# Kernel optimization log

Hardware: AMD Instinct MI355X
Metric: run time of the kernel (lower is better)

The kernel has to match this reference:

```python
import jax, jax.numpy as jnp
import numpy as np

B, S, F, RANK = 8, 4096, 1024, 64


def gram_schmidt(P):
    """Sequential Gram-Schmidt on columns of P (F, R) -> orthogonal (unnormalized) columns.
    Matches vizbert's orth_tensor: v_i = p_i - sum_{j<i} ((u_j . v)/(u_j . u_j)) u_j.
    Each step vectorizes the inner projection loop as one matmul (u_j are mutually
    orthogonal, so sequential-update and batched coefficients are equal in exact math)."""
    us = [P[:, 0]]
    for i in range(1, P.shape[1]):
        U = jnp.stack(us, axis=1)                 # (F, i)
        sq = jnp.sum(U * U, axis=0)               # (i,)
        v = P[:, i]
        coeff = (U.T @ v) / sq                    # (i,)
        us.append(v - U @ coeff)
    return jnp.stack(us, axis=1)                  # (F, R)


def setup_inputs() -> dict:
    key = jax.random.key(0)
    k1, k2 = jax.random.split(key)
    hidden_states = jax.random.normal(k1, (B, S, F), dtype=jnp.float32)
    # probe params initialized uniform(-0.05, 0.05), stacked to (num_features, rank)
    probe = jax.random.uniform(k2, (F, RANK), minval=-0.05, maxval=0.05, dtype=jnp.float32)
    return {"hidden_states": hidden_states, "probe": probe}


def reference(hidden_states, probe):
    # orth_probe: Gram-Schmidt orthogonalized probe columns (orthogonalize=True)
    U = gram_schmidt(probe)                       # (F, R), orthogonal columns
    sq = jnp.sum(U * U, axis=0)                   # (R,) squared norms

    # normalize=True: remember per-token norms before projection
    old_norms = jnp.linalg.norm(hidden_states, axis=2, keepdims=True)  # (B, S, 1)
    # mask_first=True: remember first-token states
    first_state = hidden_states[:, 0]             # (B, F)

    # full_batch_gs: subtract projection onto each probe direction.
    # Because U's columns are orthogonal, the sequential per-column subtraction
    # equals one fused projection: h - U (U^T h / ||u||^2).
    coeffs = jnp.einsum('bsf,fr->bsr', hidden_states, U) / sq
    h = hidden_states - jnp.einsum('bsr,fr->bsf', coeffs, U)

    # normalize=True: rescale back to the original per-token norm
    new_norms = jnp.linalg.norm(h, axis=2, keepdims=True)
    h = h / new_norms * old_norms

    # mask_first=True: restore the first token untouched
    h = h.at[:, 0].set(first_state)
    return h
```

## Files before the change

### kernel.cpp

```cpp
#include <hip/hip_runtime.h>


typedef __attribute__((ext_vector_type(8))) short bf16x8;
typedef __attribute__((ext_vector_type(4))) float f32x4;

#define MFMA_B16(a, b, c) __builtin_amdgcn_mfma_f32_16x16x32_bf16((a), (b), (c), 0, 0, 0)

__device__ __forceinline__ unsigned short bf16bits(float x) {
  union { float f; unsigned u; } v; v.f = x;
  return (unsigned short)((v.u + 0x7fffu + ((v.u >> 16) & 1u)) >> 16);
}

__global__ void pp_gram(const float* __restrict__ P, float* __restrict__ partial,
                        unsigned short* __restrict__ Ptb, unsigned short* __restrict__ Pb) {
  __shared__ float Pl[64][68];
  const int tid = threadIdx.x, ch = blockIdx.x;
  #pragma unroll
  for (int u = 0; u < 4; ++u) {
    const int f = tid >> 2, r = (tid & 3) * 16 + 4 * u;
    *(f32x4*)&Pl[f][r] = *(const f32x4*)(P + (size_t)(ch * 64 + f) * 64 + r);
  }
  __syncthreads();
  {
    const int f = tid >> 2, r0 = (tid & 3) * 16;
    bf16x8 w0, w1;
    #pragma unroll
    for (int j = 0; j < 8; ++j) {
      w0[j] = (short)bf16bits(Pl[f][r0 + j]);
      w1[j] = (short)bf16bits(Pl[f][r0 + 8 + j]);
    }
    *(bf16x8*)(Pb + (size_t)(ch * 64 + f) * 64 + r0) = w0;
    *(bf16x8*)(Pb + (size_t)(ch * 64 + f) * 64 + r0 + 8) = w1;
  }
  {
    const int r = tid >> 2, f0 = (tid & 3) * 16;
    bf16x8 w0, w1;
    #pragma unroll
    for (int j = 0; j < 8; ++j) {
      w0[j] = (short)bf16bits(Pl[f0 + j][r]);
      w1[j] = (short)bf16bits(Pl[f0 + 8 + j][r]);
    }
    *(bf16x8*)(Ptb + (size_t)r * 1024 + ch * 64 + f0) = w0;
    *(bf16x8*)(Ptb + (size_t)r * 1024 + ch * 64 + f0 + 8) = w1;
  }
  const int a0 = (tid >> 4) * 4, b0 = (tid & 15) * 4;
  f32x4 acc[4];
  #pragma unroll
  for (int i = 0; i < 4; ++i) acc[i] = (f32x4){0.f, 0.f, 0.f, 0.f};
  for (int k = 0; k < 64; ++k) {
    f32x4 av = *(const f32x4*)&Pl[k][a0];
    f32x4 bv = *(const f32x4*)&Pl[k][b0];
    #pragma unroll
    for (int i = 0; i < 4; ++i) acc[i] += av[i] * bv;
  }
  #pragma unroll
  for (int i = 0; i < 4; ++i)
    *(f32x4*)(partial + (size_t)ch * 4096 + (size_t)(a0 + i) * 64 + b0) = acc[i];
}

__global__ void pp_invert(const float* __restrict__ partial, unsigned short* __restrict__ Wb) {
  __shared__ float A[64][68];
  const int i = threadIdx.x;
  #pragma unroll
  for (int c = 0; c < 16; ++c) {
    f32x4 s = (f32x4){0.f, 0.f, 0.f, 0.f};
    #pragma unroll 4
    for (int p = 0; p < 16; ++p)
      s += *(const f32x4*)(partial + (size_t)p * 4096 + (size_t)i * 64 + c * 4);
    *(f32x4*)&A[i][c * 4] = s;
  }
  __syncthreads();
  for (int k = 0; k < 64; ++k) {
    const float d = 1.0f / A[k][k];
    const float fi = A[i][k];
    #pragma unroll
    for (int c = 0; c < 16; ++c) {
      f32x4 pr = *(const f32x4*)&A[k][c * 4];
      f32x4 cur = *(const f32x4*)&A[i][c * 4];
      f32x4 res;
      #pragma unroll
      for (int e = 0; e < 4; ++e) {
        const bool isp = (c * 4 + e) == k;
        const float pv = isp ? d : pr[e] * d;
        const float cu = isp ? 0.f : cur[e];
        res[e] = (i == k) ? pv : (cu - fi * pv);
      }
      *(f32x4*)&A[i][c * 4] = res;
    }
    __builtin_amdgcn_wave_barrier();
  }
  #pragma unroll
  for (int c = 0; c < 8; ++c) {
    bf16x8 w;
    #pragma unroll
    for (int j = 0; j < 8; ++j) w[j] = (short)bf16bits(A[i][c * 8 + j]);
    *(bf16x8*)(Wb + (size_t)i * 64 + c * 8) = w;
  }
}

__device__ __forceinline__ void ld_chunk(const float* __restrict__ hp, int ch, f32x4* v) {
  #pragma unroll
  for (int it = 0; it < 4; ++it) {
    v[2 * it] = *(const f32x4*)(hp + ch * 128 + it * 32);
    v[2 * it + 1] = *(const f32x4*)(hp + ch * 128 + it * 32 + 4);
  }
}

__device__ __forceinline__ void comp_chunk(const f32x4* v, const unsigned short* __restrict__ bp0,
                                           int ch, f32x4* accY, float& sqacc) {
  #pragma unroll
  for (int it = 0; it < 4; ++it) {
    const f32x4 v0 = v[2 * it], v1 = v[2 * it + 1];
    sqacc += v0[0] * v0[0] + v0[1] * v0[1] + v0[2] * v0[2] + v0[3] * v0[3] +
             v1[0] * v1[0] + v1[1] * v1[1] + v1[2] * v1[2] + v1[3] * v1[3];
    bf16x8 a;
    a[0] = (short)bf16bits(v0[0]); a[1] = (short)bf16bits(v0[1]);
    a[2] = (short)bf16bits(v0[2]); a[3] = (short)bf16bits(v0[3]);
    a[4] = (short)bf16bits(v1[0]); a[5] = (short)bf16bits(v1[1]);
    a[6] = (short)bf16bits(v1[2]); a[7] = (short)bf16bits(v1[3]);
    const unsigned short* bp = bp0 + ch * 128 + it * 32;
    #pragma unroll
    for (int t = 0; t < 4; ++t) {
      bf16x8 b = *(const bf16x8*)(bp + (size_t)t * 16 * 1024);
      accY[t] = MFMA_B16(a, b, accY[t]);
    }
  }
}

__global__ __launch_bounds__(256, 2) void pp_main(
    const float* __restrict__ H, const unsigned short* __restrict__ Ptb,
    const unsigned short* __restrict__ Pb, const unsigned short* __restrict__ Wb,
    float* __restrict__ out) {
  __shared__ __align__(16) unsigned short Yl[64][72];
  __shared__ __align__(16) unsigned short Cl[64][72];
  __shared__ __align__(16) unsigned short Wl[64][72];

  const int tid = threadIdx.x;
  const int lane = tid & 63, wid = tid >> 6;
  const int c16 = lane & 15, quad = lane >> 4;
  const int strip = wid * 16;
  const long row0 = (long)blockIdx.x * 64;

  #pragma unroll
  for (int g = 0; g < 2; ++g) {
    const int u = tid + g * 256;
    *(bf16x8*)&Wl[u >> 3][(u & 7) * 8] = *(const bf16x8*)(Wb + (size_t)u * 8);
  }
  __syncthreads();

  f32x4 accY[4];
  #pragma unroll
  for (int t = 0; t < 4; ++t) accY[t] = (f32x4){0.f, 0.f, 0.f, 0.f};
  float sqacc = 0.f;
  const float* hp = H + (row0 + strip + c16) * 1024 + quad * 8;
  const unsigned short* bp0 = Ptb + (size_t)c16 * 1024 + quad * 8;
  {
    f32x4 va[8], vb[8];
    ld_chunk(hp, 0, va);
    #pragma unroll
    for (int c2 = 0; c2 < 4; ++c2) {
      ld_chunk(hp, 2 * c2 + 1, vb);
      comp_chunk(va, bp0, 2 * c2, accY, sqacc);
      if (c2 < 3) ld_chunk(hp, 2 * c2 + 2, va);
      comp_chunk(vb, bp0, 2 * c2 + 1, accY, sqacc);
    }
  }

  sqacc += __shfl_xor(sqacc, 16);
  sqacc += __shfl_xor(sqacc, 32);

  #pragma unroll
  for (int t = 0; t < 4; ++t)
    #pragma unroll
    for (int r = 0; r < 4; ++r)
      Yl[strip + quad * 4 + r][t * 16 + c16] = bf16bits(accY[t][r]);

  f32x4 accC[4];
  #pragma unroll
  for (int t = 0; t < 4; ++t) accC[t] = (f32x4){0.f, 0.f, 0.f, 0.f};
  #pragma unroll
  for (int kk = 0; kk < 2; ++kk) {
    bf16x8 a = *(const bf16x8*)&Yl[strip + c16][kk * 32 + quad * 8];
    #pragma unroll
    for (int t = 0; t < 4; ++t) {
      bf16x8 b = *(const bf16x8*)&Wl[t * 16 + c16][kk * 32 + quad * 8];
      accC[t] = MFMA_B16(a, b, accC[t]);
    }
  }

  #pragma unroll
  for (int t = 0; t < 4; ++t)
    #pragma unroll
    for (int r = 0; r < 4; ++r)
      Cl[strip + quad * 4 + r][t * 16 + c16] = bf16bits(accC[t][r]);

  float sc[4]; long rg[4]; bool fs[4];
  #pragma unroll
  for (int r = 0; r < 4; ++r) {
    float dd = accY[0][r] * accC[0][r] + accY[1][r] * accC[1][r] +
               accY[2][r] * accC[2][r] + accY[3][r] * accC[3][r];
    dd += __shfl_xor(dd, 1);
    dd += __shfl_xor(dd, 2);
    dd += __shfl_xor(dd, 4);
    dd += __shfl_xor(dd, 8);
    const float o2 = __shfl(sqacc, quad * 4 + r);
    const float n2 = fmaxf(o2 - dd, 1e-30f);
    sc[r] = sqrtf(o2 / n2);
    rg[r] = row0 + strip + quad * 4 + r;
    fs[r] = ((rg[r] & 4095) == 0);
  }

  bf16x8 ca0 = *(const bf16x8*)&Cl[strip + c16][quad * 8];
  bf16x8 ca1 = *(const bf16x8*)&Cl[strip + c16][32 + quad * 8];
  #pragma unroll 4
  for (int ft = 0; ft < 64; ++ft) {
    const unsigned short* bp = Pb + (size_t)(ft * 16 + c16) * 64 + quad * 8;
    bf16x8 b0 = *(const bf16x8*)bp;
    bf16x8 b1 = *(const bf16x8*)(bp + 32);
    f32x4 acc = (f32x4){0.f, 0.f, 0.f, 0.f};
    acc = MFMA_B16(ca0, b0, acc);
    acc = MFMA_B16(ca1, b1, acc);
    const int f = ft * 16 + c16;
    #pragma unroll
    for (int r = 0; r < 4; ++r) {
      const long idx = rg[r] * 1024 + f;
      const float h = H[idx];
      out[idx] = fs[r] ? h : (h - acc[r]) * sc[r];
    }
  }
}

extern "C" void kernel_launch(void* const* d_in, const int* in_sizes, int n_in,
                              void* d_out, int out_size, void* d_ws, size_t ws_size,
                              hipStream_t stream) {
  const float* H = (const float*)d_in[0];
  const float* P = (const float*)d_in[1];
  float* out = (float*)d_out;
  float* partial = (float*)d_ws;
  unsigned short* Wb = (unsigned short*)(partial + 16 * 4096);
  unsigned short* Ptb = Wb + 4096;
  unsigned short* Pb = Ptb + 65536;

  pp_gram<<<16, 256, 0, stream>>>(P, partial, Ptb, Pb);
  pp_invert<<<1, 64, 0, stream>>>(partial, Wb);
  pp_main<<<512, 256, 0, stream>>>(H, Ptb, Pb, Wb, out);
}
```

Baseline: 388.8 us.

## Split-K main kernel over half-row tiles and widen Gauss-Jordan inversion to 256 threads

The main kernel now processes 32 rows per block, with two wave pairs each handling half of the feature dimension. Partial Y and squared norms are reduced through shared memory, and the output phase is split across the halves. This doubles the grid to 1024 blocks and raises the launch-bounds occupancy target to 4. The inversion kernel spreads each row across 4 threads and uses block barriers, which should shorten the serial single-wave prologue. Costs include extra LDS traffic, more __syncthreads, and half of the waves sitting idle during the small C computation.

```diff
diff --git a/kernel.cpp b/kernel.cpp
--- a/kernel.cpp
+++ b/kernel.cpp
@@ -60,41 +60,45 @@
 
 __global__ void pp_invert(const float* __restrict__ partial, unsigned short* __restrict__ Wb) {
   __shared__ float A[64][68];
-  const int i = threadIdx.x;
-  #pragma unroll
-  for (int c = 0; c < 16; ++c) {
+  const int tid = threadIdx.x;
+  const int i = tid >> 2, q16 = (tid & 3) * 16;
+  #pragma unroll
+  for (int u = 0; u < 4; ++u) {
     f32x4 s = (f32x4){0.f, 0.f, 0.f, 0.f};
-    #pragma unroll 4
-    for (int p = 0; p < 16; ++p)
-      s += *(const f32x4*)(partial + (size_t)p * 4096 + (size_t)i * 64 + c * 4);
-    *(f32x4*)&A[i][c * 4] = s;
+    const int off = i * 64 + q16 + 4 * u;
+    for (int p = 0; p < 16; ++p) s += *(const f32x4*)(partial + (size_t)p * 4096 + off);
+    *(f32x4*)&A[i][q16 + 4 * u] = s;
   }
   __syncthreads();
   for (int k = 0; k < 64; ++k) {
     const float d = 1.0f / A[k][k];
-    const float fi = A[i][k];
-    #pragma unroll
-    for (int c = 0; c < 16; ++c) {
-      f32x4 pr = *(const f32x4*)&A[k][c * 4];
-      f32x4 cur = *(const f32x4*)&A[i][c * 4];
-      f32x4 res;
-      #pragma unroll
-      for (int e = 0; e < 4; ++e) {
-        const bool isp = (c * 4 + e) == k;
-        const float pv = isp ? d : pr[e] * d;
-        const float cu = isp ? 0.f : cur[e];
-        res[e] = (i == k) ? pv : (cu - fi * pv);
-      }
-      *(f32x4*)&A[i][c * 4] = res;
-    }
-    __builtin_amdgcn_wave_barrier();
-  }
-  #pragma unroll
-  for (int c = 0; c < 8; ++c) {
-    bf16x8 w;
-    #pragma unroll
-    for (int j = 0; j < 8; ++j) w[j] = (short)bf16bits(A[i][c * 8 + j]);
-    *(bf16x8*)(Wb + (size_t)i * 64 + c * 8) = w;
+    const float f = A[i][k];
+    f32x4 prs[4], cur[4];
+    #pragma unroll
+    for (int u = 0; u < 4; ++u) {
+      prs[u] = *(const f32x4*)&A[k][q16 + 4 * u];
+      cur[u] = *(const f32x4*)&A[i][q16 + 4 * u];
+    }
+    __syncthreads();
+    const int kl = k - q16;
+    #pragma unroll
+    for (int u = 0; u < 4; ++u) {
+      f32x4 pv = prs[u] * d;
+      if (kl >= u * 4 && kl < u * 4 + 4) { pv[kl - u * 4] = d; cur[u][kl - u * 4] = 0.f; }
+      f32x4 res = (i == k) ? pv : (cur[u] - f * pv);
+      *(f32x4*)&A[i][q16 + 4 * u] = res;
+    }
+    __syncthreads();
+  }
+  {
+    bf16x8 w0, w1;
+    #pragma unroll
+    for (int j = 0; j < 8; ++j) {
+      w0[j] = (short)bf16bits(A[i][q16 + j]);
+      w1[j] = (short)bf16bits(A[i][q16 + 8 + j]);
+    }
+    *(bf16x8*)(Wb + (size_t)i * 64 + q16) = w0;
+    *(bf16x8*)(Wb + (size_t)i * 64 + q16 + 8) = w1;
   }
 }
 
@@ -127,93 +131,119 @@
   }
 }
 
-__global__ __launch_bounds__(256, 2) void pp_main(
+__global__ __launch_bounds__(256, 4) void pp_main(
     const float* __restrict__ H, const unsigned short* __restrict__ Ptb,
     const unsigned short* __restrict__ Pb, const unsigned short* __restrict__ Wb,
     float* __restrict__ out) {
-  __shared__ __align__(16) unsigned short Yl[64][72];
-  __shared__ __align__(16) unsigned short Cl[64][72];
+  __shared__ __align__(16) unsigned short Yl[32][72];
+  __shared__ __align__(16) unsigned short Cl[32][72];
   __shared__ __align__(16) unsigned short Wl[64][72];
+  __shared__ float Yp[32][68];
+  __shared__ float rs[2][32];
+  __shared__ float scalev[32];
 
   const int tid = threadIdx.x;
   const int lane = tid & 63, wid = tid >> 6;
   const int c16 = lane & 15, quad = lane >> 4;
-  const int strip = wid * 16;
-  const long row0 = (long)blockIdx.x * 64;
+  const int sw = wid & 1, kh = wid >> 1;
+  const int strip = sw * 16;
+  const long row0 = (long)blockIdx.x * 32;
 
   #pragma unroll
   for (int g = 0; g < 2; ++g) {
     const int u = tid + g * 256;
     *(bf16x8*)&Wl[u >> 3][(u & 7) * 8] = *(const bf16x8*)(Wb + (size_t)u * 8);
   }
-  __syncthreads();
 
   f32x4 accY[4];
   #pragma unroll
   for (int t = 0; t < 4; ++t) accY[t] = (f32x4){0.f, 0.f, 0.f, 0.f};
   float sqacc = 0.f;
-  const float* hp = H + (row0 + strip + c16) * 1024 + quad * 8;
-  const unsigned short* bp0 = Ptb + (size_t)c16 * 1024 + quad * 8;
+  const float* hp = H + (row0 + strip + c16) * 1024 + kh * 512 + quad * 8;
+  const unsigned short* bp0 = Ptb + (size_t)c16 * 1024 + kh * 512 + quad * 8;
   {
     f32x4 va[8], vb[8];
     ld_chunk(hp, 0, va);
-    #pragma unroll
-    for (int c2 = 0; c2 < 4; ++c2) {
-      ld_chunk(hp, 2 * c2 + 1, vb);
-      comp_chunk(va, bp0, 2 * c2, accY, sqacc);
-      if (c2 < 3) ld_chunk(hp, 2 * c2 + 2, va);
-      comp_chunk(vb, bp0, 2 * c2 + 1, accY, sqacc);
-    }
+    ld_chunk(hp, 1, vb);
+    comp_chunk(va, bp0, 0, accY, sqacc);
+    ld_chunk(hp, 2, va);
+    comp_chunk(vb, bp0, 1, accY, sqacc);
+    ld_chunk(hp, 3, vb);
+    comp_chunk(va, bp0, 2, accY, sqacc);
+    comp_chunk(vb, bp0, 3, accY, sqacc);
   }
 
   sqacc += __shfl_xor(sqacc, 16);
   sqacc += __shfl_xor(sqacc, 32);
-
-  #pragma unroll
-  for (int t = 0; t < 4; ++t)
-    #pragma unroll
-    for (int r = 0; r < 4; ++r)
-      Yl[strip + quad * 4 + r][t * 16 + c16] = bf16bits(accY[t][r]);
-
-  f32x4 accC[4];
-  #pragma unroll
-  for (int t = 0; t < 4; ++t) accC[t] = (f32x4){0.f, 0.f, 0.f, 0.f};
-  #pragma unroll
-  for (int kk = 0; kk < 2; ++kk) {
-    bf16x8 a = *(const bf16x8*)&Yl[strip + c16][kk * 32 + quad * 8];
-    #pragma unroll
-    for (int t = 0; t < 4; ++t) {
-      bf16x8 b = *(const bf16x8*)&Wl[t * 16 + c16][kk * 32 + quad * 8];
-      accC[t] = MFMA_B16(a, b, accC[t]);
-    }
-  }
-
-  #pragma unroll
-  for (int t = 0; t < 4; ++t)
-    #pragma unroll
-    for (int r = 0; r < 4; ++r)
-      Cl[strip + quad * 4 + r][t * 16 + c16] = bf16bits(accC[t][r]);
-
-  float sc[4]; long rg[4]; bool fs[4];
-  #pragma unroll
-  for (int r = 0; r < 4; ++r) {
-    float dd = accY[0][r] * accC[0][r] + accY[1][r] * accC[1][r] +
-               accY[2][r] * accC[2][r] + accY[3][r] * accC[3][r];
-    dd += __shfl_xor(dd, 1);
-    dd += __shfl_xor(dd, 2);
-    dd += __shfl_xor(dd, 4);
-    dd += __shfl_xor(dd, 8);
-    const float o2 = __shfl(sqacc, quad * 4 + r);
-    const float n2 = fmaxf(o2 - dd, 1e-30f);
-    sc[r] = sqrtf(o2 / n2);
-    rg[r] = row0 + strip + quad * 4 + r;
-    fs[r] = ((rg[r] & 4095) == 0);
-  }
+  if (quad == 0) rs[kh][strip + c16] = sqacc;
+
+  if (kh) {
+    #pragma unroll
+    for (int t = 0; t < 4; ++t)
+      #pragma unroll
+      for (int r = 0; r < 4; ++r)
+        Yp[strip + quad * 4 + r][t * 16 + c16] = accY[t][r];
+  }
+  __syncthreads();
+
+  if (kh == 0) {
+    #pragma unroll
+    for (int t = 0; t < 4; ++t)
+      #pragma unroll
+      for (int r = 0; r < 4; ++r) {
+        accY[t][r] += Yp[strip + quad * 4 + r][t * 16 + c16];
+        Yl[strip + quad * 4 + r][t * 16 + c16] = bf16bits(accY[t][r]);
+      }
+
+    f32x4 accC[4];
+    #pragma unroll
+    for (int t = 0; t < 4; ++t) accC[t] = (f32x4){0.f, 0.f, 0.f, 0.f};
+    #pragma unroll
+    for (int kk = 0; kk < 2; ++kk) {
+      bf16x8 a = *(const bf16x8*)&Yl[strip + c16][kk * 32 + quad * 8];
+      #pragma unroll
+      for (int t = 0; t < 4; ++t) {
+        bf16x8 b = *(const bf16x8*)&Wl[t * 16 + c16][kk * 32 + quad * 8];
+        accC[t] = MFMA_B16(a, b, accC[t]);
+      }
+    }
+    #pragma unroll
+    for (int t = 0; t < 4; ++t)
+      #pragma unroll
+      for (int r = 0; r < 4; ++r)
+        Cl[strip + quad * 4 + r][t * 16 + c16] = bf16bits(accC[t][r]);
+
+    #pragma unroll
+    for (int r = 0; r < 4; ++r) {
+      float dd = accY[0][r] * accC[0][r] + accY[1][r] * accC[1][r] +
+                 accY[2][r] * accC[2][r] + accY[3][r] * accC[3][r];
+      dd += __shfl_xor(dd, 1);
+      dd += __shfl_xor(dd, 2);
+      dd += __shfl_xor(dd, 4);
+      dd += __shfl_xor(dd, 8);
+      if (c16 == 0) {
+        const int row = strip + quad * 4 + r;
+        const float o2 = rs[0][row] + rs[1][row];
+        const float n2 = fmaxf(o2 - dd, 1e-30f);
+        scalev[row] = sqrtf(o2 / n2);
+      }
+    }
+  }
+  __syncthreads();
 
   bf16x8 ca0 = *(const bf16x8*)&Cl[strip + c16][quad * 8];
   bf16x8 ca1 = *(const bf16x8*)&Cl[strip + c16][32 + quad * 8];
+  float sc[4]; long rg[4]; bool fs[4];
+  #pragma unroll
+  for (int r = 0; r < 4; ++r) {
+    const int m = strip + quad * 4 + r;
+    sc[r] = scalev[m];
+    rg[r] = row0 + m;
+    fs[r] = ((rg[r] & 4095) == 0);
+  }
   #pragma unroll 4
-  for (int ft = 0; ft < 64; ++ft) {
+  for (int j = 0; j < 32; ++j) {
+    const int ft = kh * 32 + j;
     const unsigned short* bp = Pb + (size_t)(ft * 16 + c16) * 64 + quad * 8;
     bf16x8 b0 = *(const bf16x8*)bp;
     bf16x8 b1 = *(const bf16x8*)(bp + 32);
@@ -242,6 +272,6 @@
   unsigned short* Pb = Ptb + 65536;
 
   pp_gram<<<16, 256, 0, stream>>>(P, partial, Ptb, Pb);
-  pp_invert<<<1, 64, 0, stream>>>(partial, Wb);
-  pp_main<<<512, 256, 0, stream>>>(H, Ptb, Pb, Wb, out);
-}
+  pp_invert<<<1, 256, 0, stream>>>(partial, Wb);
+  pp_main<<<1024, 256, 0, stream>>>(H, Ptb, Pb, Wb, out);
+}
```

After: 326.3 us. 1.19x faster.
